# Optimization experiments

Hardware: AMD Instinct MI355X
Metric: run time of the kernel (lower is better)

## Reference

```python
import jax, jax.numpy as jnp
import numpy as np

EPS = 1e-8
ITERS = 4
NEG = -1e9

def build_grid(H, W):
    y = jnp.linspace(-1.0, 1.0, H)
    x = jnp.linspace(-1.0, 1.0, W)
    yy, xx = jnp.meshgrid(y, x, indexing='ij')
    return jnp.stack([xx, yy], axis=-1)[None]  # (1,H,W,2)

def ln(x, g, b):
    m = jnp.mean(x, -1, keepdims=True)
    v = jnp.mean(jnp.square(x - m), -1, keepdims=True)
    return (x - m) * jax.lax.rsqrt(v + 1e-5) * g + b

def gru(x, h, wih, whh, bih, bhh):
    gi = x @ wih.T + bih
    gh = h @ whh.T + bhh
    ir, iz, inn = jnp.split(gi, 3, -1)
    hr, hz, hn = jnp.split(gh, 3, -1)
    r = jax.nn.sigmoid(ir + hr)
    z = jax.nn.sigmoid(iz + hz)
    n = jnp.tanh(inn + r * hn)
    return (1.0 - z) * n + z * h


def setup_inputs():
    B, H, W, C, D, K = 4, 128, 128, 64, 64, 4
    keys = iter(jax.random.split(jax.random.key(0), 64))
    def nrm(shape, s):
        return jax.random.normal(next(keys), shape, jnp.float32) * s
    sw = C ** -0.5
    sd = D ** -0.5
    inp = dict(
        feat=nrm((B, H, W, C), 1.0),
        mask=jax.random.randint(next(keys), (K, 1, H, W), 0, 2).astype(jnp.float32),
        noise_fg=nrm((B, K, D), 1.0),
        noise_bg=nrm((B, 1, D), 1.0),
        slots_mu=nrm((1, 1, D), 1.0),
        slots_logsigma=nrm((1, 1, D), 0.1),
        slots_mu_bg=nrm((1, 1, D), 1.0),
        slots_logsigma_bg=nrm((1, 1, D), 0.1),
        norm_feat_g=jnp.ones((C,)), norm_feat_b=jnp.zeros((C,)),
        grid_embed_w=nrm((C, 4), 0.5), grid_embed_b=jnp.zeros((C,)),
        k_fg_w=nrm((C, C), sw), v_fg_w=nrm((C, C), sw),
        k_bg_w=nrm((C, C), sw), v_bg_w=nrm((C, C), sw),
        mlp_fg_ln_g=jnp.ones((C,)), mlp_fg_ln_b=jnp.zeros((C,)),
        mlp_fg_w=nrm((D, C), sw), mlp_fg_b=jnp.zeros((D,)),
        mlp_bg_ln_g=jnp.ones((C,)), mlp_bg_ln_b=jnp.zeros((C,)),
        mlp_bg_w=nrm((D, C), sw), mlp_bg_b=jnp.zeros((D,)),
        q_ln_g=jnp.ones((D,)), q_ln_b=jnp.zeros((D,)), q_w=nrm((D, D), sd),
        qbg_ln_g=jnp.ones((D,)), qbg_ln_b=jnp.zeros((D,)), qbg_w=nrm((D, D), sd),
        gru_fg_wih=nrm((3 * D, D), sd), gru_fg_whh=nrm((3 * D, D), sd),
        gru_fg_bih=jnp.zeros((3 * D,)), gru_fg_bhh=jnp.zeros((3 * D,)),
        gru_bg_wih=nrm((3 * D, D), sd), gru_bg_whh=nrm((3 * D, D), sd),
        gru_bg_bih=jnp.zeros((3 * D,)), gru_bg_bhh=jnp.zeros((3 * D,)),
        res_fg_ln_g=jnp.ones((D,)), res_fg_ln_b=jnp.zeros((D,)),
        res_fg_w=nrm((D, D), sd), res_fg_b=jnp.zeros((D,)),
        res_bg_ln_g=jnp.ones((D,)), res_bg_ln_b=jnp.zeros((D,)),
        res_bg_w=nrm((D, D), sd), res_bg_b=jnp.zeros((D,)),
    )
    return inp


def reference(feat, mask, noise_fg, noise_bg, slots_mu, slots_logsigma,
              slots_mu_bg, slots_logsigma_bg, norm_feat_g, norm_feat_b,
              grid_embed_w, grid_embed_b, k_fg_w, v_fg_w, k_bg_w, v_bg_w,
              mlp_fg_ln_g, mlp_fg_ln_b, mlp_fg_w, mlp_fg_b,
              mlp_bg_ln_g, mlp_bg_ln_b, mlp_bg_w, mlp_bg_b,
              q_ln_g, q_ln_b, q_w, qbg_ln_g, qbg_ln_b, qbg_w,
              gru_fg_wih, gru_fg_whh, gru_fg_bih, gru_fg_bhh,
              gru_bg_wih, gru_bg_whh, gru_bg_bih, gru_bg_bhh,
              res_fg_ln_g, res_fg_ln_b, res_fg_w, res_fg_b,
              res_bg_ln_g, res_bg_ln_b, res_bg_w, res_bg_b):
    B, H, W, C = feat.shape
    N = H * W
    K = mask.shape[0]
    D = slots_mu.shape[-1]
    scale = D ** -0.5
    grid = build_grid(H, W)            # (1,H,W,2)
    grid_flat = grid.reshape(N, 2)
    feat = feat.reshape(B, N, C)
    # slot init (noise passed in for determinism)
    slot_fg = slots_mu + jnp.exp(slots_logsigma) * noise_fg       # (B,K,D)
    slot_bg = slots_mu_bg + jnp.exp(slots_logsigma_bg) * noise_bg  # (B,1,D)
    # fg positions = mask-weighted grid mean
    gk = jnp.transpose(grid[0], (2, 0, 1))[None]  # (1,2,H,W)
    fg_pos = (gk * mask).sum((2, 3)) / (mask.sum((1, 2, 3))[:, None] + 1e-5)  # (K,2)
    fg_pos = jnp.broadcast_to(fg_pos[None], (B, K, 2))
    feat = ln(feat, norm_feat_g, norm_feat_b)
    # background k,v (position-independent, computed once)
    rel_bg = jnp.concatenate([grid, -grid], -1).reshape(1, 1, N, 4)
    ge_bg = rel_bg @ grid_embed_w.T + grid_embed_b                # (1,1,N,C)
    kb = (feat @ k_bg_w.T)[:, None] + ge_bg                       # (B,1,N,C)
    vb = (feat @ v_bg_w.T)[:, None] + ge_bg
    k_bg = ln(kb, mlp_bg_ln_g, mlp_bg_ln_b) @ mlp_bg_w.T + mlp_bg_b
    v_bg = ln(vb, mlp_bg_ln_g, mlp_bg_ln_b) @ mlp_bg_w.T + mlp_bg_b
    mask_flat = mask.reshape(K, N)
    kf = feat @ k_fg_w.T   # iteration-invariant input projections
    vf = feat @ v_fg_w.T
    for _ in range(ITERS):
        prev_fg, prev_bg = slot_fg, slot_bg
        q_fg = ln(slot_fg, q_ln_g, q_ln_b) @ q_w.T
        q_bg = ln(slot_bg, qbg_ln_g, qbg_ln_b) @ qbg_w.T
        # position-relative grid embedding -> per-slot k,v
        rel = grid[:, None] - fg_pos[:, :, None, None, :]          # (B,K,H,W,2)
        rel = jnp.concatenate([rel, -rel], -1).reshape(B, K, N, 4)
        ge = rel @ grid_embed_w.T + grid_embed_b                   # (B,K,N,C)
        k = ln(kf[:, None] + ge, mlp_fg_ln_g, mlp_fg_ln_b) @ mlp_fg_w.T + mlp_fg_b
        v = ln(vf[:, None] + ge, mlp_fg_ln_g, mlp_fg_ln_b) @ mlp_fg_w.T + mlp_fg_b
        # background update
        attn_bg = jax.nn.softmax(jnp.einsum('bd,bnd->bn', q_bg[:, 0], k_bg[:, 0]) * scale, axis=1) + EPS
        upd_bg = jnp.einsum('bn,bnd->bd', attn_bg, v_bg[:, 0])
        sbg = gru(upd_bg, slot_bg[:, 0], gru_bg_wih, gru_bg_whh, gru_bg_bih, gru_bg_bhh)[:, None]
        slot_bg = ln(sbg, res_bg_ln_g, res_bg_ln_b) @ res_bg_w.T + res_bg_b + prev_bg
        # foreground update (vectorized over K slots)
        logits = jnp.einsum('bkd,bknd->bkn', q_fg, k) * scale
        logits = jnp.where(mask_flat[None] == 0, NEG, logits)
        attn = jax.nn.softmax(logits, axis=-1)
        upd_fg = jnp.einsum('bkn,bknd->bkd', attn, v)
        fg_pos = jnp.einsum('bkn,nd->bkd', attn, grid_flat)
        sfg = gru(upd_fg.reshape(-1, D), slot_fg.reshape(-1, D),
                  gru_fg_wih, gru_fg_whh, gru_fg_bih, gru_fg_bhh).reshape(B, K, D)
        slot_fg = ln(sfg, res_fg_ln_g, res_fg_ln_b) @ res_fg_w.T + res_fg_b + prev_fg
    slots = jnp.concatenate([slot_bg, slot_fg], axis=1)  # (B,K+1,D)
    return slots, fg_pos
```

## Files before the change

kernel.cpp:

```cpp
#include <hip/hip_runtime.h>
#include <math.h>

#define DEVI __device__ __forceinline__

constexpr int Bb = 4, Nn = 16384, Kk = 4;
constexpr int NCH = 64;
constexpr int CH = 256;
constexpr int FG_BLK = Bb * NCH;
constexpr int NBG = 64;
constexpr int BG_BLK = Bb * NBG;
constexpr int FG_PS = 72;
constexpr int BG_PS = 130;

typedef __attribute__((ext_vector_type(8))) short bf16x8;
typedef __attribute__((ext_vector_type(8))) unsigned short u16x8;
typedef __attribute__((ext_vector_type(4))) unsigned short u16x4;
typedef __attribute__((ext_vector_type(4))) float f32x4;

DEVI float bf2f(unsigned short u){ unsigned int x = ((unsigned int)u) << 16; return __builtin_bit_cast(float, x); }
DEVI unsigned short f2bf(float f){
  unsigned int u = __builtin_bit_cast(unsigned int, f);
  u += 0x7fffu + ((u >> 16) & 1u);
  return (unsigned short)(u >> 16);
}
DEVI float rsum_16_32(float v){ v += __shfl_xor(v,16); v += __shfl_xor(v,32); return v; }
DEVI float rmax_16_32(float v){ v = fmaxf(v,__shfl_xor(v,16)); v = fmaxf(v,__shfl_xor(v,32)); return v; }
DEVI float rsum_1_8(float v){ v += __shfl_xor(v,1); v += __shfl_xor(v,2); v += __shfl_xor(v,4); v += __shfl_xor(v,8); return v; }
DEVI float rmax_1_8(float v){ v = fmaxf(v,__shfl_xor(v,1)); v = fmaxf(v,__shfl_xor(v,2)); v = fmaxf(v,__shfl_xor(v,4)); v = fmaxf(v,__shfl_xor(v,8)); return v; }
DEVI float rsum_all(float v){ return rsum_16_32(rsum_1_8(v)); }
DEVI float rmax_all(float v){ return rmax_16_32(rmax_1_8(v)); }
DEVI float sel4(float a0, float a1, float a2, float a3, int r){
  float v = a0; v = (r == 1) ? a1 : v; v = (r == 2) ? a2 : v; v = (r == 3) ? a3 : v; return v;
}
DEVI float sigm(float x){ return 1.f / (1.f + __expf(-x)); }

constexpr float GSTEP = 2.0f / 127.0f;
DEVI float gxf(int n){ return (float)(n & 127) * GSTEP - 1.0f; }
DEVI float gyf(int n){ return (float)((n >> 7) & 127) * GSTEP - 1.0f; }

#define NEGINF (-__builtin_inff())

__global__ __launch_bounds__(1024) void k_setup(
    const float* __restrict__ mask,
    const float* __restrict__ gw, const float* __restrict__ gb,
    const float* __restrict__ g_fg, const float* __restrict__ bln_fg,
    const float* __restrict__ w_fg, const float* __restrict__ b_fg,
    float* __restrict__ fg_pos, float* __restrict__ cbuf)
{
  int t = threadIdx.x;
  if (blockIdx.x < 4) {
    int k = blockIdx.x;
    const float4* mp = (const float4*)(mask + (size_t)k * Nn);
    float sm = 0, sx = 0, sy = 0;
    #pragma unroll
    for (int i = 0; i < 4; ++i) {
      int idx = t + i * 1024;
      float4 v = mp[idx];
      int n = idx * 4;
      float gy = gyf(n);
      float rowsum = v.x + v.y + v.z + v.w;
      sm += rowsum;
      sx += v.x * gxf(n) + v.y * gxf(n + 1) + v.z * gxf(n + 2) + v.w * gxf(n + 3);
      sy += rowsum * gy;
    }
    sm = rsum_all(sm); sx = rsum_all(sx); sy = rsum_all(sy);
    __shared__ float red[3][16];
    int wv = t >> 6, l = t & 63;
    if (l == 0) { red[0][wv] = sm; red[1][wv] = sx; red[2][wv] = sy; }
    __syncthreads();
    if (t == 0) {
      float S = 0, X = 0, Y = 0;
      #pragma unroll
      for (int i = 0; i < 16; ++i) { S += red[0][i]; X += red[1][i]; Y += red[2][i]; }
      float inv = 1.f / (S + 1e-5f);
      float px = X * inv, py = Y * inv;
      for (int b = 0; b < 4; ++b) { fg_pos[(b*4+k)*2+0] = px; fg_pos[(b*4+k)*2+1] = py; }
    }
  } else {
    if (t < 64) {
      float gx_t = gw[t*4+0] - gw[t*4+2];
      float gy_t = gw[t*4+1] - gw[t*4+3];
      float aGx = 0, aGy = 0, agW = 0, aC0 = 0;
      for (int c = 0; c < 64; ++c) {
        float wv = w_fg[t*64 + c];
        float gc = g_fg[c];
        float gxc = gw[c*4+0] - gw[c*4+2];
        float gyc = gw[c*4+1] - gw[c*4+3];
        aGx += gxc * gc * wv;
        aGy += gyc * gc * wv;
        agW += gc * wv;
        aC0 += bln_fg[c] * wv;
      }
      cbuf[t] = aGx; cbuf[64+t] = aGy; cbuf[128+t] = agW; cbuf[192+t] = aC0 + b_fg[t];
      float mgx = rsum_all(gx_t) * (1.f/64.f);
      float mgy = rsum_all(gy_t) * (1.f/64.f);
      float egx2 = rsum_all(gx_t*gx_t) * (1.f/64.f);
      float egy2 = rsum_all(gy_t*gy_t) * (1.f/64.f);
      float egxy = rsum_all(gx_t*gy_t) * (1.f/64.f);
      if (t == 0) { cbuf[256]=mgx; cbuf[257]=mgy; cbuf[258]=egx2; cbuf[259]=egy2; cbuf[260]=egxy; }
    }
  }
}

__global__ __launch_bounds__(256) void k_prep(
    const float* __restrict__ feat,
    const float* __restrict__ norm_g, const float* __restrict__ norm_b,
    const float* __restrict__ gw, const float* __restrict__ gb,
    const float* __restrict__ k_fg_w, const float* __restrict__ v_fg_w,
    const float* __restrict__ k_bg_w, const float* __restrict__ v_bg_w,
    const float* __restrict__ mlp_bg_ln_g, const float* __restrict__ mlp_bg_ln_b,
    const float* __restrict__ mlp_bg_w, const float* __restrict__ mlp_bg_b,
    const float* __restrict__ mlp_fg_ln_g, const float* __restrict__ mlp_fg_w,
    unsigned short* __restrict__ A_k, unsigned short* __restrict__ A_vT,
    float* __restrict__ statsKV,
    unsigned short* __restrict__ kbg, unsigned short* __restrict__ vbg,
    const float* __restrict__ noise_fg, const float* __restrict__ noise_bg,
    const float* __restrict__ mu, const float* __restrict__ ls,
    const float* __restrict__ mub, const float* __restrict__ lsb,
    const float* __restrict__ q_ln_g, const float* __restrict__ q_ln_b, const float* __restrict__ q_w,
    const float* __restrict__ qbg_ln_g, const float* __restrict__ qbg_ln_b, const float* __restrict__ qbg_w,
    const float* __restrict__ cbuf,
    float* slot_fg, float* slot_bg, float* q_fg, float* q_bg, float* qscal)
{
  int tid = threadIdx.x, wave = tid >> 6, l = tid & 63;
  if ((int)blockIdx.x >= 512) {
    __shared__ float lds[64];
    int ib = blockIdx.x - 512;
    float lnv = 0.f;
    if (tid < 64) {
      if (ib < 16) {
        float s = mu[tid] + expf(ls[tid]) * noise_fg[ib * 64 + tid];
        slot_fg[ib * 64 + tid] = s;
        float mean = rsum_all(s) * (1.f / 64.f);
        float d = s - mean;
        float var = rsum_all(d * d) * (1.f / 64.f);
        lnv = d * rsqrtf(var + 1e-5f) * q_ln_g[tid] + q_ln_b[tid];
      } else {
        int b = ib - 16;
        float s = mub[tid] + expf(lsb[tid]) * noise_bg[b * 64 + tid];
        slot_bg[b * 64 + tid] = s;
        float mean = rsum_all(s) * (1.f / 64.f);
        float d = s - mean;
        float var = rsum_all(d * d) * (1.f / 64.f);
        lnv = d * rsqrtf(var + 1e-5f) * qbg_ln_g[tid] + qbg_ln_b[tid];
      }
      lds[tid] = lnv;
    }
    __syncthreads();
    if (tid < 64) {
      if (ib < 16) {
        float acc = 0.f;
        #pragma unroll 8
        for (int c = 0; c < 64; ++c) acc += q_w[tid * 64 + c] * lds[c];
        q_fg[ib * 64 + tid] = acc;
        float qGx = rsum_all(acc * cbuf[tid]);
        float qGy = rsum_all(acc * cbuf[64 + tid]);
        float qgW = rsum_all(acc * cbuf[128 + tid]);
        float qC0 = rsum_all(acc * cbuf[192 + tid]);
        if (tid == 0) { qscal[ib*4+0]=qGx; qscal[ib*4+1]=qGy; qscal[ib*4+2]=qgW; qscal[ib*4+3]=qC0; }
      } else {
        int b = ib - 16;
        float acc = 0.f;
        #pragma unroll 8
        for (int c = 0; c < 64; ++c) acc += qbg_w[tid * 64 + c] * lds[c];
        q_bg[b * 64 + tid] = acc;
      }
    }
    return;
  }
  __shared__ bf16x8 wfrag[6 * 8 * 64];
  __shared__ __align__(16) unsigned short tbuf[4][16][88];
  __shared__ float s_gwx[64], s_gwy[64], s_gb[64], s_mlg[64], s_mlb[64], s_mbb[64], s_gf[64];
  const float* wsrc[6] = { k_fg_w, v_fg_w, k_bg_w, v_bg_w, mlp_bg_w, mlp_fg_w };
  for (int mi = wave; mi < 6; mi += 4) {
    const float* ws = wsrc[mi];
    #pragma unroll
    for (int f = 0; f < 8; ++f) {
      int ct = f >> 1, kh = f & 1;
      int row = ct * 16 + (l & 15);
      int c0 = ((l >> 4) << 3) + kh * 32;
      bf16x8 v;
      #pragma unroll
      for (int j = 0; j < 8; ++j) v[j] = (short)f2bf(ws[row * 64 + c0 + j]);
      wfrag[(mi * 8 + f) * 64 + l] = v;
    }
  }
  if (tid < 64) {
    s_gwx[tid] = gw[tid*4+0] - gw[tid*4+2];
    s_gwy[tid] = gw[tid*4+1] - gw[tid*4+3];
    s_gb[tid]  = gb[tid];
    s_mlg[tid] = mlp_bg_ln_g[tid];
    s_mlb[tid] = mlp_bg_ln_b[tid];
    s_mbb[tid] = mlp_bg_b[tid];
    s_gf[tid]  = mlp_fg_ln_g[tid];
  }
  __syncthreads();

  int cb = (l >> 4) << 3;
  float ngr[16], nbr[16];
  #pragma unroll
  for (int j = 0; j < 16; ++j) {
    int col = (j < 8) ? (cb + j) : (32 + cb + j - 8);
    ngr[j] = norm_g[col]; nbr[j] = norm_b[col];
  }
  float gwxD[4], gwyD[4], gbD[4], mlgD[4], mlbD[4], mbbD[4], gfD[4];
  #pragma unroll
  for (int ct = 0; ct < 4; ++ct) {
    int col = ct * 16 + (l & 15);
    gwxD[ct] = s_gwx[col]; gwyD[ct] = s_gwy[col]; gbD[ct] = s_gb[col];
    mlgD[ct] = s_mlg[col]; mlbD[ct] = s_mlb[col]; mbbD[ct] = s_mbb[col];
    gfD[ct] = s_gf[col];
  }

  int wg = blockIdx.x * 4 + wave;
  for (int tt = 0; tt < 2; ++tt) {
    int tile = wg * 2 + tt;
    int rowg = tile * 16 + (l & 15);
    const float* fp = feat + (size_t)rowg * 64;
    float x[16];
    #pragma unroll
    for (int j = 0; j < 8; ++j) x[j] = fp[cb + j];
    #pragma unroll
    for (int j = 0; j < 8; ++j) x[8 + j] = fp[32 + cb + j];
    float sm = 0;
    #pragma unroll
    for (int j = 0; j < 16; ++j) sm += x[j];
    float mean = rsum_16_32(sm) * (1.f / 64.f);
    float vv = 0;
    #pragma unroll
    for (int j = 0; j < 16; ++j) { float d = x[j] - mean; vv += d * d; }
    float rstd = rsqrtf(rsum_16_32(vv) * (1.f / 64.f) + 1e-5f);
    bf16x8 a0, a1;
    #pragma unroll
    for (int j = 0; j < 8; ++j) a0[j] = (short)f2bf((x[j] - mean) * rstd * ngr[j] + nbr[j]);
    #pragma unroll
    for (int j = 0; j < 8; ++j) a1[j] = (short)f2bf((x[8 + j] - mean) * rstd * ngr[8 + j] + nbr[8 + j]);

    for (int mi = 0; mi < 4; ++mi) {
      f32x4 acc[4];
      #pragma unroll
      for (int ct = 0; ct < 4; ++ct) acc[ct] = (f32x4){0.f, 0.f, 0.f, 0.f};
      #pragma unroll
      for (int ct = 0; ct < 4; ++ct) {
        acc[ct] = __builtin_amdgcn_mfma_f32_16x16x32_bf16(a0, wfrag[(mi * 8 + ct * 2 + 0) * 64 + l], acc[ct], 0, 0, 0);
        acc[ct] = __builtin_amdgcn_mfma_f32_16x16x32_bf16(a1, wfrag[(mi * 8 + ct * 2 + 1) * 64 + l], acc[ct], 0, 0, 0);
      }
      if (mi < 2) {
        #pragma unroll
        for (int ct = 0; ct < 4; ++ct)
          #pragma unroll
          for (int r = 0; r < 4; ++r)
            acc[ct][r] += gbD[ct];
        float s1[4], s2[4], sx[4], sy[4];
        #pragma unroll
        for (int r = 0; r < 4; ++r) {
          float a0v = acc[0][r], a1v = acc[1][r], a2v = acc[2][r], a3v = acc[3][r];
          s1[r] = rsum_1_8(a0v + a1v + a2v + a3v);
          s2[r] = rsum_1_8(a0v*a0v + a1v*a1v + a2v*a2v + a3v*a3v);
          sx[r] = rsum_1_8(a0v*gwxD[0] + a1v*gwxD[1] + a2v*gwxD[2] + a3v*gwxD[3]);
          sy[r] = rsum_1_8(a0v*gwyD[0] + a1v*gwyD[1] + a2v*gwyD[2] + a3v*gwyD[3]);
        }
        int rsel = l & 15;
        if (rsel < 4) {
          float4 stv;
          stv.x = sel4(s1[0], s1[1], s1[2], s1[3], rsel) * (1.f/64.f);
          stv.y = sel4(s2[0], s2[1], s2[2], s2[3], rsel) * (1.f/64.f);
          stv.z = sel4(sx[0], sx[1], sx[2], sx[3], rsel) * (1.f/64.f);
          stv.w = sel4(sy[0], sy[1], sy[2], sy[3], rsel) * (1.f/64.f);
          int frow = tile * 16 + (l >> 4) * 4 + rsel;
          *(float4*)(statsKV + (size_t)frow * 8 + mi * 4) = stv;
        }
        #pragma unroll
        for (int ct = 0; ct < 4; ++ct)
          #pragma unroll
          for (int r = 0; r < 4; ++r)
            tbuf[wave][(l >> 4) * 4 + r][ct * 16 + (l & 15)] = f2bf(acc[ct][r] * gfD[ct]);
        bf16x8 b0 = *(const bf16x8*)&tbuf[wave][l & 15][cb];
        bf16x8 b1 = *(const bf16x8*)&tbuf[wave][l & 15][32 + cb];
        f32x4 acc2[4];
        #pragma unroll
        for (int ct = 0; ct < 4; ++ct) acc2[ct] = (f32x4){0.f, 0.f, 0.f, 0.f};
        #pragma unroll
        for (int ct = 0; ct < 4; ++ct) {
          acc2[ct] = __builtin_amdgcn_mfma_f32_16x16x32_bf16(b0, wfrag[(5 * 8 + ct * 2 + 0) * 64 + l], acc2[ct], 0, 0, 0);
          acc2[ct] = __builtin_amdgcn_mfma_f32_16x16x32_bf16(b1, wfrag[(5 * 8 + ct * 2 + 1) * 64 + l], acc2[ct], 0, 0, 0);
        }
        if (mi == 0) {
          #pragma unroll
          for (int ct = 0; ct < 4; ++ct)
            #pragma unroll
            for (int r = 0; r < 4; ++r)
              tbuf[wave][(l >> 4) * 4 + r][ct * 16 + (l & 15)] = f2bf(acc2[ct][r]);
          u16x8 o0 = *(const u16x8*)&tbuf[wave][l & 15][cb];
          u16x8 o1 = *(const u16x8*)&tbuf[wave][l & 15][32 + cb];
          *(u16x8*)(A_k + (size_t)rowg * 64 + cb) = o0;
          *(u16x8*)(A_k + (size_t)rowg * 64 + 32 + cb) = o1;
        } else {
          int bb = tile >> 10;
          int nb4 = (tile * 16 + ((l >> 4) << 2)) & (Nn - 1);
          #pragma unroll
          for (int ct = 0; ct < 4; ++ct) {
            u16x4 u4;
            u4[0] = f2bf(acc2[ct][0]); u4[1] = f2bf(acc2[ct][1]);
            u4[2] = f2bf(acc2[ct][2]); u4[3] = f2bf(acc2[ct][3]);
            int d = ct * 16 + (l & 15);
            *(u16x4*)(A_vT + ((size_t)bb * 64 + d) * Nn + nb4) = u4;
          }
        }
      } else {
        #pragma unroll
        for (int ct = 0; ct < 4; ++ct)
          #pragma unroll
          for (int r = 0; r < 4; ++r) {
            int n = (tile * 16 + (l >> 4) * 4 + r) & (Nn - 1);
            acc[ct][r] += gwxD[ct] * gxf(n) + gwyD[ct] * gyf(n) + gbD[ct];
          }
        float mrow[4], rstd2[4];
        #pragma unroll
        for (int r = 0; r < 4; ++r) {
          float srow = acc[0][r] + acc[1][r] + acc[2][r] + acc[3][r];
          srow = rsum_1_8(srow);
          mrow[r] = srow * (1.f / 64.f);
          float vr = 0;
          #pragma unroll
          for (int ct = 0; ct < 4; ++ct) { float d = acc[ct][r] - mrow[r]; vr += d * d; }
          vr = rsum_1_8(vr);
          rstd2[r] = rsqrtf(vr * (1.f / 64.f) + 1e-5f);
        }
        #pragma unroll
        for (int ct = 0; ct < 4; ++ct)
          #pragma unroll
          for (int r = 0; r < 4; ++r)
            tbuf[wave][(l >> 4) * 4 + r][ct * 16 + (l & 15)] =
                f2bf((acc[ct][r] - mrow[r]) * rstd2[r] * mlgD[ct] + mlbD[ct]);
        bf16x8 b0 = *(const bf16x8*)&tbuf[wave][l & 15][cb];
        bf16x8 b1 = *(const bf16x8*)&tbuf[wave][l & 15][32 + cb];
        f32x4 acc2[4];
        #pragma unroll
        for (int ct = 0; ct < 4; ++ct) acc2[ct] = (f32x4){0.f, 0.f, 0.f, 0.f};
        #pragma unroll
        for (int ct = 0; ct < 4; ++ct) {
          acc2[ct] = __builtin_amdgcn_mfma_f32_16x16x32_bf16(b0, wfrag[(4 * 8 + ct * 2 + 0) * 64 + l], acc2[ct], 0, 0, 0);
          acc2[ct] = __builtin_amdgcn_mfma_f32_16x16x32_bf16(b1, wfrag[(4 * 8 + ct * 2 + 1) * 64 + l], acc2[ct], 0, 0, 0);
        }
        #pragma unroll
        for (int ct = 0; ct < 4; ++ct)
          #pragma unroll
          for (int r = 0; r < 4; ++r)
            tbuf[wave][(l >> 4) * 4 + r][ct * 16 + (l & 15)] = f2bf(acc2[ct][r] + mbbD[ct]);
        unsigned short* dst = (mi == 2) ? kbg : vbg;
        u16x8 o0 = *(const u16x8*)&tbuf[wave][l & 15][cb];
        u16x8 o1 = *(const u16x8*)&tbuf[wave][l & 15][32 + cb];
        *(u16x8*)(dst + (size_t)rowg * 64 + cb) = o0;
        *(u16x8*)(dst + (size_t)rowg * 64 + 32 + cb) = o1;
      }
    }
  }
}

__global__ __launch_bounds__(256) void k_iter(
    const unsigned short* __restrict__ A_k, const unsigned short* __restrict__ A_vT,
    const float* __restrict__ statsKV,
    const unsigned short* __restrict__ kbg, const unsigned short* __restrict__ vbg,
    const float* __restrict__ q_fg, const float* __restrict__ q_bg,
    const float* __restrict__ fg_pos, const float* __restrict__ mask,
    const float* __restrict__ cbuf, const float* __restrict__ qscal,
    float* __restrict__ fgP, float* __restrict__ bgP)
{
  __shared__ float qa_pl[4][260];
  __shared__ __align__(16) unsigned short w_buf[4][272];
  __shared__ float redv[4][4][64];
  __shared__ float shred[4][130];
  int tid = threadIdx.x, wave = tid >> 6, l = tid & 63;
  if ((int)blockIdx.x < FG_BLK) {
    int b = blockIdx.x >> 6, ch = blockIdx.x & 63;
    int n0 = ch * CH;
    int slot = l & 15;
    bf16x8 qf0, qf1;
    {
      int bkq = b * 4 + (slot & 3);
      #pragma unroll
      for (int j = 0; j < 8; ++j) {
        float v0 = q_fg[bkq * 64 + (l >> 4) * 8 + j];
        float v1 = q_fg[bkq * 64 + 32 + (l >> 4) * 8 + j];
        qf0[j] = (short)f2bf(slot < 4 ? v0 : 0.f);
        qf1[j] = (short)f2bf(slot < 4 ? v1 : 0.f);
      }
    }
    #pragma unroll
    for (int tt2 = 0; tt2 < 4; ++tt2) {
      int t = wave * 4 + tt2;
      const unsigned short* ap = A_k + ((size_t)b * Nn + n0 + t * 16 + (l & 15)) * 64 + ((l >> 4) << 3);
      bf16x8 b0 = *(const bf16x8*)ap;
      bf16x8 b1 = *(const bf16x8*)(ap + 32);
      f32x4 acc = (f32x4){0.f, 0.f, 0.f, 0.f};
      acc = __builtin_amdgcn_mfma_f32_16x16x32_bf16(qf0, b0, acc, 0, 0, 0);
      acc = __builtin_amdgcn_mfma_f32_16x16x32_bf16(qf1, b1, acc, 0, 0, 0);
      if (l < 16) {
        #pragma unroll
        for (int r = 0; r < 4; ++r) qa_pl[r][t * 16 + l] = acc[r];
      }
    }
    __syncthreads();
    int w = wave;
    float pxw = fg_pos[(b * 4 + w) * 2 + 0], pyw = fg_pos[(b * 4 + w) * 2 + 1];
    float qGx = qscal[(b*4+w)*4+0], qGy = qscal[(b*4+w)*4+1];
    float qgW = qscal[(b*4+w)*4+2], qC0 = qscal[(b*4+w)*4+3];
    float mgx = cbuf[256], mgy = cbuf[257], egx2 = cbuf[258], egy2 = cbuf[259], egxy = cbuf[260];
    float lgc[4], rsv[4], muvc[4];
    float mx = NEGINF;
    #pragma unroll
    for (int i = 0; i < 4; ++i) {
      int n = n0 + i * 64 + l;
      const float* st = statsKV + ((size_t)b * Nn + n) * 8;
      float4 sk = *(const float4*)st;
      float4 sv = *(const float4*)(st + 4);
      float gx = gxf(n), gy = gyf(n);
      float relx = gx - pxw, rely = gy - pyw;
      float mu = sk.x + relx * mgx + rely * mgy;
      float ex2 = sk.y + 2.f*(relx*sk.z + rely*sk.w) + relx*relx*egx2 + rely*rely*egy2 + 2.f*relx*rely*egxy;
      float rstd = rsqrtf(fmaxf(ex2 - mu * mu, 0.f) + 1e-5f);
      float qa = qa_pl[w][i * 64 + l];
      float lg = 0.125f * (rstd * (qa + relx * qGx + rely * qGy - mu * qgW) + qC0);
      float mk = mask[w * Nn + n];
      lg = (mk == 0.f) ? -1e9f : lg;
      lgc[i] = lg; mx = fmaxf(mx, lg);
      float muv = sv.x + relx * mgx + rely * mgy;
      float ex2v = sv.y + 2.f*(relx*sv.z + rely*sv.w) + relx*relx*egx2 + rely*rely*egy2 + 2.f*relx*rely*egxy;
      rsv[i] = rsqrtf(fmaxf(ex2v - muv * muv, 0.f) + 1e-5f);
      muvc[i] = muv;
    }
    float mb = rmax_all(mx);
    float s_a = 0, px_a = 0, py_a = 0, swx = 0, swy = 0, swm = 0;
    #pragma unroll
    for (int i = 0; i < 4; ++i) {
      int n = n0 + i * 64 + l;
      float e = __expf(lgc[i] - mb);
      float gx = gxf(n), gy = gyf(n);
      s_a += e; px_a += e * gx; py_a += e * gy;
      float wgt = e * rsv[i];
      swx += wgt * (gx - pxw); swy += wgt * (gy - pyw); swm += wgt * muvc[i];
      w_buf[w][i * 64 + l] = f2bf(wgt);
    }
    s_a = rsum_all(s_a); px_a = rsum_all(px_a); py_a = rsum_all(py_a);
    swx = rsum_all(swx); swy = rsum_all(swy); swm = rsum_all(swm);
    if (l == 0) {
      float* P = fgP + ((size_t)(b * NCH + ch) * 4 + w) * FG_PS;
      P[0] = mb; P[1] = s_a; P[2] = px_a; P[3] = py_a; P[4] = swx; P[5] = swy; P[6] = swm;
    }
    __syncthreads();
    f32x4 acc[4];
    #pragma unroll
    for (int ct = 0; ct < 4; ++ct) acc[ct] = (f32x4){0.f, 0.f, 0.f, 0.f};
    bf16x8 zz;
    #pragma unroll
    for (int j = 0; j < 8; ++j) zz[j] = 0;
    #pragma unroll
    for (int st2 = 0; st2 < 2; ++st2) {
      int noff = wave * 64 + st2 * 32;
      bf16x8 wf = *(const bf16x8*)&w_buf[l & 3][noff + ((l >> 4) << 3)];
      if ((l & 15) >= 4) wf = zz;
      #pragma unroll
      for (int ct = 0; ct < 4; ++ct) {
        const unsigned short* ap = A_vT + ((size_t)b * 64 + ct * 16 + (l & 15)) * Nn + n0 + noff + ((l >> 4) << 3);
        bf16x8 bv = *(const bf16x8*)ap;
        acc[ct] = __builtin_amdgcn_mfma_f32_16x16x32_bf16(wf, bv, acc[ct], 0, 0, 0);
      }
    }
    if (l < 16) {
      #pragma unroll
      for (int ct = 0; ct < 4; ++ct)
        #pragma unroll
        for (int r = 0; r < 4; ++r)
          redv[wave][r][ct * 16 + l] = acc[ct][r];
    }
    __syncthreads();
    if (wave == 0) {
      #pragma unroll
      for (int s2 = 0; s2 < 4; ++s2) {
        float v = redv[0][s2][l] + redv[1][s2][l] + redv[2][s2][l] + redv[3][s2][l];
        fgP[((size_t)(b * NCH + ch) * 4 + s2) * FG_PS + 8 + l] = v;
      }
    }
  } else {
    int idx = blockIdx.x - FG_BLK;
    int b = idx >> 6, nb = idx & 63;
    int cb16 = (l >> 4) << 4;
    float qr[16];
    #pragma unroll
    for (int i = 0; i < 16; ++i) qr[i] = q_bg[b * 64 + cb16 + i];
    float m = NEGINF, s = 0.f, upd[16], sv[16];
    #pragma unroll
    for (int i = 0; i < 16; ++i) { upd[i] = 0; sv[i] = 0; }
    #pragma unroll
    for (int pass = 0; pass < 4; ++pass) {
      int nrow = nb * 256 + pass * 64 + wave * 16 + (l & 15);
      const unsigned short* kp = kbg + ((size_t)b * Nn + nrow) * 64 + cb16;
      const unsigned short* vp = vbg + ((size_t)b * Nn + nrow) * 64 + cb16;
      u16x8 k0 = *(const u16x8*)kp, k1 = *(const u16x8*)(kp + 8);
      u16x8 v0 = *(const u16x8*)vp, v1 = *(const u16x8*)(vp + 8);
      float p = 0;
      #pragma unroll
      for (int i = 0; i < 8; ++i) { p += qr[i] * bf2f(k0[i]); p += qr[8 + i] * bf2f(k1[i]); }
      p = rsum_16_32(p);
      float lg = 0.125f * p;
      float tm = rmax_1_8(lg);
      float mnew = fmaxf(m, tm);
      float alpha = __expf(m - mnew); m = mnew;
      s *= alpha;
      #pragma unroll
      for (int i = 0; i < 16; ++i) upd[i] *= alpha;
      float e = __expf(lg - mnew);
      s += e;
      #pragma unroll
      for (int i = 0; i < 8; ++i) {
        float fv0 = bf2f(v0[i]), fv1 = bf2f(v1[i]);
        upd[i] += e * fv0; upd[8 + i] += e * fv1;
        sv[i] += fv0; sv[8 + i] += fv1;
      }
    }
    s = rsum_1_8(s);
    #pragma unroll
    for (int i = 0; i < 16; ++i) { upd[i] = rsum_1_8(upd[i]); sv[i] = rsum_1_8(sv[i]); }
    if (l == 0) { shred[wave][0] = m; shred[wave][1] = s; }
    if ((l & 15) == 0) {
      int g = l >> 4;
      #pragma unroll
      for (int i = 0; i < 16; ++i) { shred[wave][2 + g * 16 + i] = upd[i]; shred[wave][66 + g * 16 + i] = sv[i]; }
    }
    __syncthreads();
    if (wave == 0) {
      float m0 = shred[0][0], m1 = shred[1][0], m2 = shred[2][0], m3 = shred[3][0];
      float mg = fmaxf(fmaxf(m0, m1), fmaxf(m2, m3));
      float w0 = __expf(m0 - mg), w1 = __expf(m1 - mg), w2 = __expf(m2 - mg), w3 = __expf(m3 - mg);
      float* P = bgP + (size_t)idx * BG_PS;
      P[2 + l]  = w0 * shred[0][2 + l] + w1 * shred[1][2 + l] + w2 * shred[2][2 + l] + w3 * shred[3][2 + l];
      P[66 + l] = shred[0][66 + l] + shred[1][66 + l] + shred[2][66 + l] + shred[3][66 + l];
      if (l == 0) {
        P[0] = mg;
        P[1] = w0 * shred[0][1] + w1 * shred[1][1] + w2 * shred[2][1] + w3 * shred[3][1];
      }
    }
  }
}

__global__ __launch_bounds__(256) void k_comb(
    const float* __restrict__ fgP, const float* __restrict__ bgP,
    float* slot_fg, float* slot_bg,
    float* q_fg, float* q_bg, float* fg_pos, float* qscal,
    const float* __restrict__ cbuf,
    const float* __restrict__ gru_fg_wih, const float* __restrict__ gru_fg_whh,
    const float* __restrict__ gru_fg_bih, const float* __restrict__ gru_fg_bhh,
    const float* __restrict__ gru_bg_wih, const float* __restrict__ gru_bg_whh,
    const float* __restrict__ gru_bg_bih, const float* __restrict__ gru_bg_bhh,
    const float* __restrict__ res_fg_ln_g, const float* __restrict__ res_fg_ln_b,
    const float* __restrict__ res_fg_w, const float* __restrict__ res_fg_b,
    const float* __restrict__ res_bg_ln_g, const float* __restrict__ res_bg_ln_b,
    const float* __restrict__ res_bg_w, const float* __restrict__ res_bg_b,
    const float* __restrict__ q_ln_g, const float* __restrict__ q_ln_b, const float* __restrict__ q_w,
    const float* __restrict__ qbg_ln_g, const float* __restrict__ qbg_ln_b, const float* __restrict__ qbg_w,
    float* __restrict__ dout)
{
  __shared__ float wl[64];
  __shared__ float ubuf[4][64];
  __shared__ float part[4][64];
  __shared__ float xs[64], hs[64];
  __shared__ float gd[384];
  __shared__ float scal[6];
  int tid = threadIdx.x, wv = tid >> 6, l = tid & 63;
  int blk = blockIdx.x;
  if (blk < 16) {
    int bk = blk, b = bk >> 2, k = bk & 3;
    if (wv == 0) {
      const float* pp = fgP + ((size_t)(b * NCH + l) * 4 + k) * FG_PS;
      float mp = pp[0];
      float sp = pp[1];
      float pxp = pp[2];
      float pyp = pp[3];
      float sxp = pp[4];
      float syp = pp[5];
      float smp = pp[6];
      float mg = rmax_all(mp);
      float w = __expf(mp - mg);
      wl[l] = w;
      float S = rsum_all(w * sp);
      float px = rsum_all(w * pxp);
      float py = rsum_all(w * pyp);
      float sxg = rsum_all(w * sxp);
      float syg = rsum_all(w * syp);
      float smg = rsum_all(w * smp);
      if (l == 0) { scal[0]=S; scal[1]=px/S; scal[2]=py/S; scal[3]=sxg; scal[4]=syg; scal[5]=smg; }
    }
    __syncthreads();
    float S = scal[0];
    float acc = 0;
    #pragma unroll
    for (int i = 0; i < 16; ++i) {
      int c = wv * 16 + i;
      acc += wl[c] * fgP[((size_t)(b * NCH + c) * 4 + k) * FG_PS + 8 + l];
    }
    ubuf[wv][l] = acc;
    __syncthreads();
    if (wv == 0) {
      float UV = ubuf[0][l] + ubuf[1][l] + ubuf[2][l] + ubuf[3][l];
      float upd = (UV + scal[3] * cbuf[l] + scal[4] * cbuf[64 + l] - scal[5] * cbuf[128 + l]) / S + cbuf[192 + l];
      xs[l] = upd;
      hs[l] = slot_fg[bk * 64 + l];
    }
    __syncthreads();
    {
      int r = tid;
      float a;
      if (r < 192) {
        const float* w = gru_fg_wih + r * 64; a = gru_fg_bih[r];
        #pragma unroll 8
        for (int c = 0; c < 64; ++c) a += w[c] * xs[c];
      } else {
        const float* w = gru_fg_whh + (r - 192) * 64; a = gru_fg_bhh[r - 192];
        #pragma unroll 8
        for (int c = 0; c < 64; ++c) a += w[c] * hs[c];
      }
      gd[r] = a;
      if (tid < 128) {
        int r2 = tid + 256;
        const float* w = gru_fg_whh + (r2 - 192) * 64; float a2 = gru_fg_bhh[r2 - 192];
        #pragma unroll 8
        for (int c = 0; c < 64; ++c) a2 += w[c] * hs[c];
        gd[r2] = a2;
      }
    }
    __syncthreads();
    if (wv == 0) {
      float h = hs[l];
      float r = sigm(gd[l] + gd[192 + l]);
      float z = sigm(gd[64 + l] + gd[256 + l]);
      float nng = tanhf(gd[128 + l] + r * gd[320 + l]);
      float hnew = (1.f - z) * nng + z * h;
      float mean = rsum_all(hnew) * (1.f / 64.f);
      float d = hnew - mean;
      float var = rsum_all(d * d) * (1.f / 64.f);
      xs[l] = d * rsqrtf(var + 1e-5f) * res_fg_ln_g[l] + res_fg_ln_b[l];
    }
    __syncthreads();
    {
      int c0 = wv * 16;
      const float* w = res_fg_w + l * 64 + c0;
      float a = 0;
      #pragma unroll
      for (int c = 0; c < 16; ++c) a += w[c] * xs[c0 + c];
      part[wv][l] = a;
    }
    __syncthreads();
    if (wv == 0) {
      float h = hs[l];
      float snew = part[0][l] + part[1][l] + part[2][l] + part[3][l] + res_fg_b[l] + h;
      slot_fg[bk * 64 + l] = snew;
      dout[(b * 5 + 1 + k) * 64 + l] = snew;
      float mq = rsum_all(snew) * (1.f / 64.f);
      float dq = snew - mq;
      float vq = rsum_all(dq * dq) * (1.f / 64.f);
      xs[l] = dq * rsqrtf(vq + 1e-5f) * q_ln_g[l] + q_ln_b[l];
    }
    __syncthreads();
    {
      int c0 = wv * 16;
      const float* w = q_w + l * 64 + c0;
      float a = 0;
      #pragma unroll
      for (int c = 0; c < 16; ++c) a += w[c] * xs[c0 + c];
      part[wv][l] = a;
    }
    __syncthreads();
    if (wv == 0) {
      float qacc = part[0][l] + part[1][l] + part[2][l] + part[3][l];
      q_fg[bk * 64 + l] = qacc;
      float qGx = rsum_all(qacc * cbuf[l]);
      float qGy = rsum_all(qacc * cbuf[64 + l]);
      float qgW = rsum_all(qacc * cbuf[128 + l]);
      float qC0 = rsum_all(qacc * cbuf[192 + l]);
      if (l == 0) {
        qscal[bk*4+0]=qGx; qscal[bk*4+1]=qGy; qscal[bk*4+2]=qgW; qscal[bk*4+3]=qC0;
        float px = scal[1], py = scal[2];
        fg_pos[bk * 2 + 0] = px; fg_pos[bk * 2 + 1] = py;
        dout[1280 + bk * 2 + 0] = px; dout[1280 + bk * 2 + 1] = py;
      }
    }
  } else {
    int b = blk - 16;
    const float* P = bgP + (size_t)b * NBG * BG_PS;
    if (wv == 0) {
      float mp = P[l * BG_PS + 0];
      float sp = P[l * BG_PS + 1];
      float mg = rmax_all(mp);
      float w = __expf(mp - mg);
      wl[l] = w;
      float S = rsum_all(w * sp);
      if (l == 0) scal[0] = S;
    }
    __syncthreads();
    float S = scal[0];
    float acc = 0, sva = 0;
    #pragma unroll
    for (int i = 0; i < 16; ++i) {
      int p = wv * 16 + i;
      acc += wl[p] * P[(size_t)p * BG_PS + 2 + l];
      sva += P[(size_t)p * BG_PS + 66 + l];
    }
    ubuf[wv][l] = acc; part[wv][l] = sva;
    __syncthreads();
    if (wv == 0) {
      float upd = (ubuf[0][l] + ubuf[1][l] + ubuf[2][l] + ubuf[3][l]) / S
                + 1e-8f * (part[0][l] + part[1][l] + part[2][l] + part[3][l]);
      xs[l] = upd;
      hs[l] = slot_bg[b * 64 + l];
    }
    __syncthreads();
    {
      int r = tid;
      float a;
      if (r < 192) {
        const float* w = gru_bg_wih + r * 64; a = gru_bg_bih[r];
        #pragma unroll 8
        for (int c = 0; c < 64; ++c) a += w[c] * xs[c];
      } else {
        const float* w = gru_bg_whh + (r - 192) * 64; a = gru_bg_bhh[r - 192];
        #pragma unroll 8
        for (int c = 0; c < 64; ++c) a += w[c] * hs[c];
      }
      gd[r] = a;
      if (tid < 128) {
        int r2 = tid + 256;
        const float* w = gru_bg_whh + (r2 - 192) * 64; float a2 = gru_bg_bhh[r2 - 192];
        #pragma unroll 8
        for (int c = 0; c < 64; ++c) a2 += w[c] * hs[c];
        gd[r2] = a2;
      }
    }
    __syncthreads();
    if (wv == 0) {
      float h = hs[l];
      float r = sigm(gd[l] + gd[192 + l]);
      float z = sigm(gd[64 + l] + gd[256 + l]);
      float nng = tanhf(gd[128 + l] + r * gd[320 + l]);
      float hnew = (1.f - z) * nng + z * h;
      float mean = rsum_all(hnew) * (1.f / 64.f);
      float d = hnew - mean;
      float var = rsum_all(d * d) * (1.f / 64.f);
      xs[l] = d * rsqrtf(var + 1e-5f) * res_bg_ln_g[l] + res_bg_ln_b[l];
    }
    __syncthreads();
    {
      int c0 = wv * 16;
      const float* w = res_bg_w + l * 64 + c0;
      float a = 0;
      #pragma unroll
      for (int c = 0; c < 16; ++c) a += w[c] * xs[c0 + c];
      part[wv][l] = a;
    }
    __syncthreads();
    if (wv == 0) {
      float h = hs[l];
      float snew = part[0][l] + part[1][l] + part[2][l] + part[3][l] + res_bg_b[l] + h;
      slot_bg[b * 64 + l] = snew;
      dout[(b * 5 + 0) * 64 + l] = snew;
      float mq = rsum_all(snew) * (1.f / 64.f);
      float dq = snew - mq;
      float vq = rsum_all(dq * dq) * (1.f / 64.f);
      xs[l] = dq * rsqrtf(vq + 1e-5f) * qbg_ln_g[l] + qbg_ln_b[l];
    }
    __syncthreads();
    {
      int c0 = wv * 16;
      const float* w = qbg_w + l * 64 + c0;
      float a = 0;
      #pragma unroll
      for (int c = 0; c < 16; ++c) a += w[c] * xs[c0 + c];
      part[wv][l] = a;
    }
    __syncthreads();
    if (wv == 0) {
      q_bg[b * 64 + l] = part[0][l] + part[1][l] + part[2][l] + part[3][l];
    }
  }
}

extern "C" void kernel_launch(void* const* d_in, const int* in_sizes, int n_in,
                              void* d_out, int out_size, void* d_ws, size_t ws_size,
                              hipStream_t stream)
{
  (void)in_sizes; (void)n_in; (void)out_size; (void)ws_size;
  const float* feat        = (const float*)d_in[0];
  const float* mask        = (const float*)d_in[1];
  const float* noise_fg    = (const float*)d_in[2];
  const float* noise_bg    = (const float*)d_in[3];
  const float* slots_mu    = (const float*)d_in[4];
  const float* slots_ls    = (const float*)d_in[5];
  const float* slots_mu_bg = (const float*)d_in[6];
  const float* slots_ls_bg = (const float*)d_in[7];
  const float* norm_feat_g = (const float*)d_in[8];
  const float* norm_feat_b = (const float*)d_in[9];
  const float* grid_embed_w= (const float*)d_in[10];
  const float* grid_embed_b= (const float*)d_in[11];
  const float* k_fg_w      = (const float*)d_in[12];
  const float* v_fg_w      = (const float*)d_in[13];
  const float* k_bg_w      = (const float*)d_in[14];
  const float* v_bg_w      = (const float*)d_in[15];
  const float* mlp_fg_ln_g = (const float*)d_in[16];
  const float* mlp_fg_ln_b = (const float*)d_in[17];
  const float* mlp_fg_w    = (const float*)d_in[18];
  const float* mlp_fg_b    = (const float*)d_in[19];
  const float* mlp_bg_ln_g = (const float*)d_in[20];
  const float* mlp_bg_ln_b = (const float*)d_in[21];
  const float* mlp_bg_w    = (const float*)d_in[22];
  const float* mlp_bg_b    = (const float*)d_in[23];
  const float* q_ln_g      = (const float*)d_in[24];
  const float* q_ln_b      = (const float*)d_in[25];
  const float* q_w         = (const float*)d_in[26];
  const float* qbg_ln_g    = (const float*)d_in[27];
  const float* qbg_ln_b    = (const float*)d_in[28];
  const float* qbg_w       = (const float*)d_in[29];
  const float* gru_fg_wih  = (const float*)d_in[30];
  const float* gru_fg_whh  = (const float*)d_in[31];
  const float* gru_fg_bih  = (const float*)d_in[32];
  const float* gru_fg_bhh  = (const float*)d_in[33];
  const float* gru_bg_wih  = (const float*)d_in[34];
  const float* gru_bg_whh  = (const float*)d_in[35];
  const float* gru_bg_bih  = (const float*)d_in[36];
  const float* gru_bg_bhh  = (const float*)d_in[37];
  const float* res_fg_ln_g = (const float*)d_in[38];
  const float* res_fg_ln_b = (const float*)d_in[39];
  const float* res_fg_w    = (const float*)d_in[40];
  const float* res_fg_b    = (const float*)d_in[41];
  const float* res_bg_ln_g = (const float*)d_in[42];
  const float* res_bg_ln_b = (const float*)d_in[43];
  const float* res_bg_w    = (const float*)d_in[44];
  const float* res_bg_b    = (const float*)d_in[45];
  float* dout = (float*)d_out;

  char* wsp = (char*)d_ws;
  size_t off = 0;
  auto alloc = [&](size_t bytes) -> void* {
    void* p = wsp + off;
    off += (bytes + 255) & ~(size_t)255;
    return p;
  };
  unsigned short* A_k  = (unsigned short*)alloc((size_t)Bb * Nn * 64 * 2);
  unsigned short* A_vT = (unsigned short*)alloc((size_t)Bb * Nn * 64 * 2);
  float* statsKV       = (float*)alloc((size_t)Bb * Nn * 8 * 4);
  unsigned short* kbg  = (unsigned short*)alloc((size_t)Bb * Nn * 64 * 2);
  unsigned short* vbg  = (unsigned short*)alloc((size_t)Bb * Nn * 64 * 2);
  float* slot_fg = (float*)alloc(16 * 64 * 4);
  float* slot_bg = (float*)alloc(4 * 64 * 4);
  float* q_fg    = (float*)alloc(16 * 64 * 4);
  float* q_bg    = (float*)alloc(4 * 64 * 4);
  float* fg_pos  = (float*)alloc(16 * 2 * 4);
  float* qscal   = (float*)alloc(16 * 4 * 4);
  float* cbuf    = (float*)alloc(264 * 4);
  float* fgP     = (float*)alloc((size_t)Bb * NCH * 4 * FG_PS * 4);
  float* bgP     = (float*)alloc((size_t)BG_BLK * BG_PS * 4);

  k_setup<<<5, 1024, 0, stream>>>(mask, grid_embed_w, grid_embed_b, mlp_fg_ln_g, mlp_fg_ln_b,
                                  mlp_fg_w, mlp_fg_b, fg_pos, cbuf);
  k_prep<<<532, 256, 0, stream>>>(feat, norm_feat_g, norm_feat_b, grid_embed_w, grid_embed_b,
                                  k_fg_w, v_fg_w, k_bg_w, v_bg_w,
                                  mlp_bg_ln_g, mlp_bg_ln_b, mlp_bg_w, mlp_bg_b,
                                  mlp_fg_ln_g, mlp_fg_w,
                                  A_k, A_vT, statsKV, kbg, vbg,
                                  noise_fg, noise_bg, slots_mu, slots_ls, slots_mu_bg, slots_ls_bg,
                                  q_ln_g, q_ln_b, q_w, qbg_ln_g, qbg_ln_b, qbg_w, cbuf,
                                  slot_fg, slot_bg, q_fg, q_bg, qscal);
  for (int it = 0; it < 4; ++it) {
    k_iter<<<FG_BLK + BG_BLK, 256, 0, stream>>>(A_k, A_vT, statsKV, kbg, vbg,
                                                q_fg, q_bg, fg_pos, mask, cbuf, qscal,
                                                fgP, bgP);
    k_comb<<<20, 256, 0, stream>>>(fgP, bgP, slot_fg, slot_bg, q_fg, q_bg, fg_pos, qscal, cbuf,
                                   gru_fg_wih, gru_fg_whh, gru_fg_bih, gru_fg_bhh,
                                   gru_bg_wih, gru_bg_whh, gru_bg_bih, gru_bg_bhh,
                                   res_fg_ln_g, res_fg_ln_b, res_fg_w, res_fg_b,
                                   res_bg_ln_g, res_bg_ln_b, res_bg_w, res_bg_b,
                                   q_ln_g, q_ln_b, q_w, qbg_ln_g, qbg_ln_b, qbg_w,
                                   dout);
  }
}
```

Baseline: 116.8 us.

## Precompute bf16 weight fragments once and tile V-transpose layout per 16 tokens

Weight fragment conversion to bf16 moves out of every k_prep block into a single extra k_setup block that writes the fragments to global memory, and k_prep loads them into registers instead of rebuilding a 48KB LDS copy per block. A_vT is also rearranged into 16-token tiles of 64x16, so both the k_prep stores and the k_iter MFMA loads touch contiguous 2KB chunks instead of rows strided by N. The change trades per-block conversion work and LDS pressure for global or L2 weight reads and more live registers.

Result: faster. 112.8 us (-3.4%).

```diff
diff --git a/kernel.cpp b/kernel.cpp
--- a/kernel.cpp
+++ b/kernel.cpp
@@ -11,6 +11,7 @@
 constexpr int BG_BLK = Bb * NBG;
 constexpr int FG_PS = 72;
 constexpr int BG_PS = 130;
+constexpr int NT = Nn / 16;
 
 typedef __attribute__((ext_vector_type(8))) short bf16x8;
 typedef __attribute__((ext_vector_type(8))) unsigned short u16x8;
@@ -45,7 +46,11 @@
     const float* __restrict__ gw, const float* __restrict__ gb,
     const float* __restrict__ g_fg, const float* __restrict__ bln_fg,
     const float* __restrict__ w_fg, const float* __restrict__ b_fg,
-    float* __restrict__ fg_pos, float* __restrict__ cbuf)
+    const float* __restrict__ k_fg_w, const float* __restrict__ v_fg_w,
+    const float* __restrict__ k_bg_w, const float* __restrict__ v_bg_w,
+    const float* __restrict__ mlp_bg_w,
+    float* __restrict__ fg_pos, float* __restrict__ cbuf,
+    unsigned short* __restrict__ wfragG)
 {
   int t = threadIdx.x;
   if (blockIdx.x < 4) {
@@ -76,7 +81,7 @@
       float px = X * inv, py = Y * inv;
       for (int b = 0; b < 4; ++b) { fg_pos[(b*4+k)*2+0] = px; fg_pos[(b*4+k)*2+1] = py; }
     }
-  } else {
+  } else if (blockIdx.x == 4) {
     if (t < 64) {
       float gx_t = gw[t*4+0] - gw[t*4+2];
       float gy_t = gw[t*4+1] - gw[t*4+3];
@@ -99,6 +104,20 @@
       float egxy = rsum_all(gx_t*gy_t) * (1.f/64.f);
       if (t == 0) { cbuf[256]=mgx; cbuf[257]=mgy; cbuf[258]=egx2; cbuf[259]=egy2; cbuf[260]=egxy; }
     }
+  } else {
+    const float* wsrc[6] = { k_fg_w, v_fg_w, k_bg_w, v_bg_w, mlp_bg_w, w_fg };
+    for (int e = t; e < 6 * 8 * 64; e += 1024) {
+      int mi = e >> 9;
+      int f = (e >> 6) & 7;
+      int l = e & 63;
+      const float* ws = wsrc[mi];
+      int ct = f >> 1, kh = f & 1;
+      int row = ct * 16 + (l & 15);
+      int c0 = ((l >> 4) << 3) + kh * 32;
+      unsigned short* dst = wfragG + (size_t)e * 8;
+      #pragma unroll
+      for (int j = 0; j < 8; ++j) dst[j] = f2bf(ws[row * 64 + c0 + j]);
+    }
   }
 }
 
@@ -106,11 +125,9 @@
     const float* __restrict__ feat,
     const float* __restrict__ norm_g, const float* __restrict__ norm_b,
     const float* __restrict__ gw, const float* __restrict__ gb,
-    const float* __restrict__ k_fg_w, const float* __restrict__ v_fg_w,
-    const float* __restrict__ k_bg_w, const float* __restrict__ v_bg_w,
     const float* __restrict__ mlp_bg_ln_g, const float* __restrict__ mlp_bg_ln_b,
-    const float* __restrict__ mlp_bg_w, const float* __restrict__ mlp_bg_b,
-    const float* __restrict__ mlp_fg_ln_g, const float* __restrict__ mlp_fg_w,
+    const float* __restrict__ mlp_bg_b, const float* __restrict__ mlp_fg_ln_g,
+    const unsigned short* __restrict__ wfragG,
     unsigned short* __restrict__ A_k, unsigned short* __restrict__ A_vT,
     float* __restrict__ statsKV,
     unsigned short* __restrict__ kbg, unsigned short* __restrict__ vbg,
@@ -168,23 +185,8 @@
     }
     return;
   }
-  __shared__ bf16x8 wfrag[6 * 8 * 64];
   __shared__ __align__(16) unsigned short tbuf[4][16][88];
   __shared__ float s_gwx[64], s_gwy[64], s_gb[64], s_mlg[64], s_mlb[64], s_mbb[64], s_gf[64];
-  const float* wsrc[6] = { k_fg_w, v_fg_w, k_bg_w, v_bg_w, mlp_bg_w, mlp_fg_w };
-  for (int mi = wave; mi < 6; mi += 4) {
-    const float* ws = wsrc[mi];
-    #pragma unroll
-    for (int f = 0; f < 8; ++f) {
-      int ct = f >> 1, kh = f & 1;
-      int row = ct * 16 + (l & 15);
-      int c0 = ((l >> 4) << 3) + kh * 32;
-      bf16x8 v;
-      #pragma unroll
-      for (int j = 0; j < 8; ++j) v[j] = (short)f2bf(ws[row * 64 + c0 + j]);
-      wfrag[(mi * 8 + f) * 64 + l] = v;
-    }
-  }
   if (tid < 64) {
     s_gwx[tid] = gw[tid*4+0] - gw[tid*4+2];
     s_gwy[tid] = gw[tid*4+1] - gw[tid*4+3];
@@ -237,13 +239,16 @@
     for (int j = 0; j < 8; ++j) a1[j] = (short)f2bf((x[8 + j] - mean) * rstd * ngr[8 + j] + nbr[8 + j]);
 
     for (int mi = 0; mi < 4; ++mi) {
+      bf16x8 wA[8];
+      #pragma unroll
+      for (int f = 0; f < 8; ++f) wA[f] = *(const bf16x8*)(wfragG + ((size_t)(mi * 8 + f) * 64 + l) * 8);
       f32x4 acc[4];
       #pragma unroll
       for (int ct = 0; ct < 4; ++ct) acc[ct] = (f32x4){0.f, 0.f, 0.f, 0.f};
       #pragma unroll
       for (int ct = 0; ct < 4; ++ct) {
-        acc[ct] = __builtin_amdgcn_mfma_f32_16x16x32_bf16(a0, wfrag[(mi * 8 + ct * 2 + 0) * 64 + l], acc[ct], 0, 0, 0);
-        acc[ct] = __builtin_amdgcn_mfma_f32_16x16x32_bf16(a1, wfrag[(mi * 8 + ct * 2 + 1) * 64 + l], acc[ct], 0, 0, 0);
+        acc[ct] = __builtin_amdgcn_mfma_f32_16x16x32_bf16(a0, wA[ct * 2 + 0], acc[ct], 0, 0, 0);
+        acc[ct] = __builtin_amdgcn_mfma_f32_16x16x32_bf16(a1, wA[ct * 2 + 1], acc[ct], 0, 0, 0);
       }
       if (mi < 2) {
         #pragma unroll
@@ -277,13 +282,16 @@
             tbuf[wave][(l >> 4) * 4 + r][ct * 16 + (l & 15)] = f2bf(acc[ct][r] * gfD[ct]);
         bf16x8 b0 = *(const bf16x8*)&tbuf[wave][l & 15][cb];
         bf16x8 b1 = *(const bf16x8*)&tbuf[wave][l & 15][32 + cb];
+        bf16x8 wB[8];
+        #pragma unroll
+        for (int f = 0; f < 8; ++f) wB[f] = *(const bf16x8*)(wfragG + ((size_t)(5 * 8 + f) * 64 + l) * 8);
         f32x4 acc2[4];
         #pragma unroll
         for (int ct = 0; ct < 4; ++ct) acc2[ct] = (f32x4){0.f, 0.f, 0.f, 0.f};
         #pragma unroll
         for (int ct = 0; ct < 4; ++ct) {
-          acc2[ct] = __builtin_amdgcn_mfma_f32_16x16x32_bf16(b0, wfrag[(5 * 8 + ct * 2 + 0) * 64 + l], acc2[ct], 0, 0, 0);
-          acc2[ct] = __builtin_amdgcn_mfma_f32_16x16x32_bf16(b1, wfrag[(5 * 8 + ct * 2 + 1) * 64 + l], acc2[ct], 0, 0, 0);
+          acc2[ct] = __builtin_amdgcn_mfma_f32_16x16x32_bf16(b0, wB[ct * 2 + 0], acc2[ct], 0, 0, 0);
+          acc2[ct] = __builtin_amdgcn_mfma_f32_16x16x32_bf16(b1, wB[ct * 2 + 1], acc2[ct], 0, 0, 0);
         }
         if (mi == 0) {
           #pragma unroll
@@ -297,14 +305,15 @@
           *(u16x8*)(A_k + (size_t)rowg * 64 + 32 + cb) = o1;
         } else {
           int bb = tile >> 10;
-          int nb4 = (tile * 16 + ((l >> 4) << 2)) & (Nn - 1);
+          int tloc = tile & (NT - 1);
+          int offn = (l >> 4) << 2;
           #pragma unroll
           for (int ct = 0; ct < 4; ++ct) {
             u16x4 u4;
             u4[0] = f2bf(acc2[ct][0]); u4[1] = f2bf(acc2[ct][1]);
             u4[2] = f2bf(acc2[ct][2]); u4[3] = f2bf(acc2[ct][3]);
             int d = ct * 16 + (l & 15);
-            *(u16x4*)(A_vT + ((size_t)bb * 64 + d) * Nn + nb4) = u4;
+            *(u16x4*)(A_vT + (((size_t)bb * NT + tloc) * 64 + d) * 16 + offn) = u4;
           }
         }
       } else {
@@ -335,13 +344,16 @@
                 f2bf((acc[ct][r] - mrow[r]) * rstd2[r] * mlgD[ct] + mlbD[ct]);
         bf16x8 b0 = *(const bf16x8*)&tbuf[wave][l & 15][cb];
         bf16x8 b1 = *(const bf16x8*)&tbuf[wave][l & 15][32 + cb];
+        bf16x8 wB[8];
+        #pragma unroll
+        for (int f = 0; f < 8; ++f) wB[f] = *(const bf16x8*)(wfragG + ((size_t)(4 * 8 + f) * 64 + l) * 8);
         f32x4 acc2[4];
         #pragma unroll
         for (int ct = 0; ct < 4; ++ct) acc2[ct] = (f32x4){0.f, 0.f, 0.f, 0.f};
         #pragma unroll
         for (int ct = 0; ct < 4; ++ct) {
-          acc2[ct] = __builtin_amdgcn_mfma_f32_16x16x32_bf16(b0, wfrag[(4 * 8 + ct * 2 + 0) * 64 + l], acc2[ct], 0, 0, 0);
-          acc2[ct] = __builtin_amdgcn_mfma_f32_16x16x32_bf16(b1, wfrag[(4 * 8 + ct * 2 + 1) * 64 + l], acc2[ct], 0, 0, 0);
+          acc2[ct] = __builtin_amdgcn_mfma_f32_16x16x32_bf16(b0, wB[ct * 2 + 0], acc2[ct], 0, 0, 0);
+          acc2[ct] = __builtin_amdgcn_mfma_f32_16x16x32_bf16(b1, wB[ct * 2 + 1], acc2[ct], 0, 0, 0);
         }
         #pragma unroll
         for (int ct = 0; ct < 4; ++ct)
@@ -460,9 +472,10 @@
       int noff = wave * 64 + st2 * 32;
       bf16x8 wf = *(const bf16x8*)&w_buf[l & 3][noff + ((l >> 4) << 3)];
       if ((l & 15) >= 4) wf = zz;
+      int nst = n0 + noff + ((l >> 4) << 3);
       #pragma unroll
       for (int ct = 0; ct < 4; ++ct) {
-        const unsigned short* ap = A_vT + ((size_t)b * 64 + ct * 16 + (l & 15)) * Nn + n0 + noff + ((l >> 4) << 3);
+        const unsigned short* ap = A_vT + (((size_t)b * NT + (nst >> 4)) * 64 + ct * 16 + (l & 15)) * 16 + (nst & 15);
         bf16x8 bv = *(const bf16x8*)ap;
         acc[ct] = __builtin_amdgcn_mfma_f32_16x16x32_bf16(wf, bv, acc[ct], 0, 0, 0);
       }
@@ -849,6 +862,7 @@
   float* statsKV       = (float*)alloc((size_t)Bb * Nn * 8 * 4);
   unsigned short* kbg  = (unsigned short*)alloc((size_t)Bb * Nn * 64 * 2);
   unsigned short* vbg  = (unsigned short*)alloc((size_t)Bb * Nn * 64 * 2);
+  unsigned short* wfragG = (unsigned short*)alloc(6 * 8 * 64 * 8 * 2);
   float* slot_fg = (float*)alloc(16 * 64 * 4);
   float* slot_bg = (float*)alloc(4 * 64 * 4);
   float* q_fg    = (float*)alloc(16 * 64 * 4);
@@ -859,12 +873,13 @@
   float* fgP     = (float*)alloc((size_t)Bb * NCH * 4 * FG_PS * 4);
   float* bgP     = (float*)alloc((size_t)BG_BLK * BG_PS * 4);
 
-  k_setup<<<5, 1024, 0, stream>>>(mask, grid_embed_w, grid_embed_b, mlp_fg_ln_g, mlp_fg_ln_b,
-                                  mlp_fg_w, mlp_fg_b, fg_pos, cbuf);
+  k_setup<<<6, 1024, 0, stream>>>(mask, grid_embed_w, grid_embed_b, mlp_fg_ln_g, mlp_fg_ln_b,
+                                  mlp_fg_w, mlp_fg_b,
+                                  k_fg_w, v_fg_w, k_bg_w, v_bg_w, mlp_bg_w,
+                                  fg_pos, cbuf, wfragG);
   k_prep<<<532, 256, 0, stream>>>(feat, norm_feat_g, norm_feat_b, grid_embed_w, grid_embed_b,
-                                  k_fg_w, v_fg_w, k_bg_w, v_bg_w,
-                                  mlp_bg_ln_g, mlp_bg_ln_b, mlp_bg_w, mlp_bg_b,
-                                  mlp_fg_ln_g, mlp_fg_w,
+                                  mlp_bg_ln_g, mlp_bg_ln_b, mlp_bg_b, mlp_fg_ln_g,
+                                  wfragG,
                                   A_k, A_vT, statsKV, kbg, vbg,
                                   noise_fg, noise_bg, slots_mu, slots_ls, slots_mu_bg, slots_ls_bg,
                                   q_ln_g, q_ln_b, q_w, qbg_ln_g, qbg_ln_b, qbg_w, cbuf,
```
